# Optimization experiments

Measured on AMD Instinct MI355X. Metric: run time of the kernel, lower is better.

The kernel has to match this reference:

```python
import jax, jax.numpy as jnp
import numpy as np

ALPHA = 1.0
BETA = 2.0
GAMMA = 1.5  # PositionEffectFunction default (config.gamma is NOT passed through)
TEMPERATURE = 1.0


def position_matrix(L: int) -> jnp.ndarray:
    idx = jnp.arange(L, dtype=jnp.float32)
    dist = jnp.abs(idx[:, None] - idx[None, :]) / L  # normalized |i-j|/L
    base = jnp.exp(-BETA * dist)
    return ALPHA * (1.0 + GAMMA * base) / (1.0 + GAMMA)  # [L, L]


def setup_inputs() -> dict:
    key = jax.random.key(0)
    ks = jax.random.split(key, 10)
    B, S, D = 8, 2048, 1024
    std = 0.02
    return {
        "x": jax.random.normal(ks[0], (B, S, D), jnp.float32),
        "pos_emb": jax.random.normal(ks[1], (1, S, D), jnp.float32),
        "Wq": jax.random.normal(ks[2], (D, D), jnp.float32) * std,
        "bq": jax.random.normal(ks[3], (D,), jnp.float32) * std,
        "Wk": jax.random.normal(ks[4], (D, D), jnp.float32) * std,
        "bk": jax.random.normal(ks[5], (D,), jnp.float32) * std,
        "Wv": jax.random.normal(ks[6], (D, D), jnp.float32) * std,
        "bv": jax.random.normal(ks[7], (D,), jnp.float32) * std,
        "Wo": jax.random.normal(ks[8], (D, D), jnp.float32) * std,
        "bo": jax.random.normal(ks[9], (D,), jnp.float32) * std,
    }


def reference(x, pos_emb, Wq, bq, Wk, bk, Wv, bv, Wo, bo):
    B, S, D = x.shape
    x = x + pos_emb[:, :S, :]
    Q = x @ Wq + bq  # [B,S,D]
    K = x @ Wk + bk
    V = x @ Wv + bv
    scores = jnp.einsum("bsd,btd->bst", Q, K) / jnp.sqrt(jnp.float32(D))
    pw = position_matrix(S)  # [S,S], broadcast over batch
    scores = scores * pw[None, :, :] / TEMPERATURE
    attn = jax.nn.softmax(scores, axis=-1)  # [B,S,S]
    out = jnp.einsum("bst,btd->bsd", attn, V)
    out = out @ Wo + bo
    return out, attn
```

## Files before the change

kernel.cpp:

```cpp
#include <hip/hip_runtime.h>
#include <hip/hip_bf16.h>
#include <cstdint>

typedef _Float16 f16x8 __attribute__((ext_vector_type(8)));
typedef _Float16 f16x4 __attribute__((ext_vector_type(4)));
typedef float    f32x4 __attribute__((ext_vector_type(4)));

static constexpr int B = 8, S = 2048, D = 1024;
static constexpr long BSD = (long)B * S * D;
static constexpr long SD  = (long)S * D;
static constexpr long SS  = (long)S * S;
static constexpr long DD  = (long)D * D;

__device__ __forceinline__ void gload16(const void* g, void* l) {
  __builtin_amdgcn_global_load_lds(
      (const __attribute__((address_space(1))) void*)g,
      (__attribute__((address_space(3))) void*)l, 16, 0, 0);
}

#define CFENCE() asm volatile("" ::: "memory")

__global__ __launch_bounds__(256) void prep_x_kernel(
    const float* __restrict__ x, const float* __restrict__ pos,
    _Float16* __restrict__ xh) {
  long i = ((long)blockIdx.x * 256 + threadIdx.x) * 4;
  float4 xv = *(const float4*)(x + i);
  long p = i & (SD - 1);
  float4 pv = *(const float4*)(pos + p);
  f16x4 h;
  h.x = (_Float16)(xv.x + pv.x);
  h.y = (_Float16)(xv.y + pv.y);
  h.z = (_Float16)(xv.z + pv.z);
  h.w = (_Float16)(xv.w + pv.w);
  *(f16x4*)(xh + i) = h;
}

__global__ __launch_bounds__(256) void prep_w_kernel(
    const float* __restrict__ Wq, const float* __restrict__ Wk,
    const float* __restrict__ Wv, const float* __restrict__ Wo,
    _Float16* __restrict__ wqkv, _Float16* __restrict__ woh) {
  __shared__ _Float16 t[64][65];
  const int c0 = blockIdx.x * 64;
  const int r0 = blockIdx.y * 64;
  const int tid = threadIdx.x;
  const int lc = tid & 63;
  const int lr4 = tid >> 6;
  const float* srcs[4] = {Wq, Wk, Wv, Wo};
  #pragma unroll
  for (int m = 0; m < 4; ++m) {
    const float* src = srcs[m];
    _Float16* dst = (m < 3) ? (wqkv + (long)m * DD) : woh;
    #pragma unroll
    for (int ii = 0; ii < 16; ++ii) {
      int row = ii * 4 + lr4;
      t[lc][row] = (_Float16)src[(long)(r0 + row) * D + c0 + lc];
    }
    __syncthreads();
    #pragma unroll
    for (int ii = 0; ii < 16; ++ii) {
      int orow = ii * 4 + lr4;
      dst[(long)(c0 + orow) * D + r0 + lc] = t[orow][lc];
    }
    __syncthreads();
  }
}

__global__ __launch_bounds__(256) void prep_misc_kernel(
    const float* __restrict__ bq, const float* __restrict__ bk,
    const float* __restrict__ bv,
    float* __restrict__ bcat, float* __restrict__ pwtab) {
  int i = blockIdx.x * 256 + threadIdx.x;
  if (i < 3072) {
    float v = (i < 1024) ? bq[i] : (i < 2048) ? bk[i - 1024] : bv[i - 2048];
    bcat[i] = v;
  }
  int d = i - 3072;
  if (d >= 0 && d < 2048) {
    float dist = (float)d * (1.0f / 2048.0f);
    pwtab[d] = (1.0f + 1.5f * expf(-2.0f * dist)) * (1.0f / 2.5f) * (1.0f / 32.0f);
  }
}


enum { EPI_QKV = 0, EPI_SF16 = 1, EPI_PVO = 2, EPI_F32B = 3 };

__device__ __forceinline__ void stage_half(
    char* smem, const _Float16* mb, int off, int k64K, int sthb,
    int dst0, int dst1) {
  gload16(mb + off, smem + sthb + dst0);
  gload16(mb + off + k64K, smem + sthb + dst1);
}

__device__ __forceinline__ void rdA(const char* p, f16x8 (&af)[4][2]) {
#pragma unroll
  for (int mr = 0; mr < 4; ++mr)
#pragma unroll
    for (int kk = 0; kk < 2; ++kk)
      af[mr][kk] = *(const f16x8*)(p + mr * 2048 + kk * 1024);
}

__device__ __forceinline__ void rdB(const char* p, f16x8 (&bf)[2][2]) {
#pragma unroll
  for (int nr = 0; nr < 2; ++nr)
#pragma unroll
    for (int kk = 0; kk < 2; ++kk)
      bf[nr][kk] = *(const f16x8*)(p + nr * 2048 + kk * 1024);
}

__device__ __forceinline__ void mfma16(const f16x8 (&af)[4][2],
                                       const f16x8 (&bf)[2][2],
                                       f32x4 (&a4)[4][2]) {
#pragma unroll
  for (int kk = 0; kk < 2; ++kk)
#pragma unroll
    for (int mr = 0; mr < 4; ++mr)
#pragma unroll
      for (int nr = 0; nr < 2; ++nr)
        a4[mr][nr] = __builtin_amdgcn_mfma_f32_16x16x32_f16(
            af[mr][kk], bf[nr][kk], a4[mr][nr], 0, 0, 0);
}

template<int EPI>
__global__ __launch_bounds__(512, 2) void gemm256_kernel(
    const _Float16* __restrict__ A, const _Float16* __restrict__ Bt,
    const float* __restrict__ bias, const float* __restrict__ pwtab,
    float* __restrict__ outF,
    _Float16* __restrict__ o0, _Float16* __restrict__ o1, _Float16* __restrict__ o2,
    int M, int N, int K, long sA, long sB, long sC)
{
  __shared__ __align__(16) char smem[131072];
  const int tid = threadIdx.x;

  int bx = blockIdx.x, by = blockIdx.y, bz = blockIdx.z;
  if (gridDim.z == 1) {
    const int bid = by * gridDim.x + bx;
    const int idx = bid >> 3;
    by = ((bid & 7) << 3) + (idx & 7);
    bx = idx >> 3;
  } else {
    const int f = (bz * gridDim.y + by) * gridDim.x + bx;
    bz = f & 7;
    const int r = f >> 3;
    const int ri = r & 15;
    const int cid = r >> 4;
    const int cxs = gridDim.x >> 2;
    bx = (cid & (cxs - 1)) * 4 + (ri & 3);
    by = (cid / cxs) * 4 + (ri >> 2);
  }
  const int z = bz;
  const int rb = by * 256;
  const int cb = bx * 256;
  const _Float16* Ag = A + (long)z * sA + (long)rb * K;
  const _Float16* Bg = Bt + (long)z * sB + (long)cb * K;

  const int lane = tid & 63;
  const int wid = tid >> 6;
  const int lrin = lane & 15;
  const int lhi = lane >> 4;
  const int rtail = (lrin * 64 + lhi * 16) ^ (((lane >> 3) & 1) << 5);
  const int aoff = ((wid >> 2) * 4) * 2048 + rtail;
  const int boff = ((wid & 3) * 2) * 2048 + rtail;

  const int rin = lane >> 2;
  const int cinp = (lane & 3) ^ (((lane >> 5) & 1) << 1);
  const int rowc = (wid >> 1) * 16 + rin;
  const int colc = (wid & 1) * 32 + cinp * 8;
  const int stBase = rowc * K + colc;
  const int k64K = 64 * K;
  const int h128K = 128 * K;
  const int dst0 = tid * 16;
  const int dst1 = 8192 + tid * 16;

  const int NT = K >> 6;
  f32x4 acc00[4][2] = {}, acc01[4][2] = {}, acc11[4][2] = {}, acc10[4][2] = {};

  stage_half(smem, Ag, stBase,              k64K, 0,             dst0, dst1);
  stage_half(smem, Bg, stBase,              k64K, 32768,         dst0, dst1);
  stage_half(smem, Ag, stBase + h128K,      k64K, 16384,         dst0, dst1);
  stage_half(smem, Bg, stBase + h128K,      k64K, 49152,         dst0, dst1);
  stage_half(smem, Ag, stBase + 64,         k64K, 65536,         dst0, dst1);
  stage_half(smem, Bg, stBase + h128K + 64, k64K, 65536 + 49152, dst0, dst1);
  asm volatile("s_waitcnt vmcnt(4)" ::: "memory");
  __builtin_amdgcn_s_barrier();
  CFENCE();

  for (int t = 0; t < NT; ++t) {
    const int curbase = (t & 1) << 16;
    const int nxtbase = curbase ^ 65536;
    const bool s1ok = (t + 1) < NT;
    const bool s2ok = (t + 2) < NT;
    const int st1 = stBase + (t + 1) * 64;
    const int st2 = stBase + (t + 2) * 64;
    f16x8 af[4][2], bfA[2][2], bfB[2][2];

    rdA((const char*)smem + curbase + aoff, af);
    rdB((const char*)smem + curbase + 32768 + boff, bfA);
    if (s1ok) stage_half(smem, Ag, st1 + h128K, k64K, nxtbase + 16384, dst0, dst1);
    CFENCE();
    __builtin_amdgcn_s_barrier();
    CFENCE();
    __builtin_amdgcn_s_setprio(1);
    mfma16(af, bfA, acc00);
    __builtin_amdgcn_s_setprio(0);

    rdB((const char*)smem + curbase + 49152 + boff, bfB);
    if (s1ok) stage_half(smem, Bg, st1, k64K, nxtbase + 32768, dst0, dst1);
    CFENCE();
    __builtin_amdgcn_s_barrier();
    CFENCE();
    __builtin_amdgcn_s_setprio(1);
    mfma16(af, bfB, acc01);
    __builtin_amdgcn_s_setprio(0);

    rdA((const char*)smem + curbase + 16384 + aoff, af);
    if (s2ok) stage_half(smem, Ag, st2, k64K, curbase + 0, dst0, dst1);
    CFENCE();
    __builtin_amdgcn_s_barrier();
    CFENCE();
    __builtin_amdgcn_s_setprio(1);
    mfma16(af, bfB, acc11);
    __builtin_amdgcn_s_setprio(0);

    rdB((const char*)smem + curbase + 32768 + boff, bfA);
    if (s2ok) stage_half(smem, Bg, st2 + h128K, k64K, curbase + 49152, dst0, dst1);
    if (s2ok) {
      asm volatile("s_waitcnt vmcnt(4)" ::: "memory");
    } else {
      asm volatile("s_waitcnt vmcnt(0)" ::: "memory");
    }
    CFENCE();
    __builtin_amdgcn_s_barrier();
    CFENCE();
    __builtin_amdgcn_s_setprio(1);
    mfma16(af, bfA, acc10);
    __builtin_amdgcn_s_setprio(0);
  }

  const int wrow = (wid >> 2) * 64;
  const int wcol = (wid & 3) * 32;
  const int matid = (EPI == EPI_QKV) ? (cb >> 10) : 0;

  if (EPI == EPI_F32B) {
    auto epi = [&](const f32x4 (&a4)[4][2], int qm, int qn) {
#pragma unroll
      for (int nr = 0; nr < 2; ++nr) {
        const int col = cb + qn * 128 + wcol + nr * 16 + lrin;
        const float bv = bias[col];
#pragma unroll
        for (int mr = 0; mr < 4; ++mr) {
          const int rowb = rb + qm * 128 + wrow + mr * 16 + lhi * 4;
          const f32x4 v4 = a4[mr][nr];
#pragma unroll
          for (int r = 0; r < 4; ++r)
            outF[(long)(rowb + r) * N + col] = v4[r] + bv;
        }
      }
    };
    epi(acc00, 0, 0);
    epi(acc01, 0, 1);
    epi(acc11, 1, 1);
    epi(acc10, 1, 0);
  } else if (EPI == EPI_QKV && matid == 2) {
    __syncthreads();
    auto vfrag = [&](const f32x4 (&a4)[4][2], int qm, int qn) {
#pragma unroll
      for (int nr = 0; nr < 2; ++nr) {
        const int dl = qn * 128 + wcol + nr * 16 + lrin;
        const float bv = bias[cb + dl];
        const int xr = (dl & 7) << 4;
#pragma unroll
        for (int mr = 0; mr < 4; ++mr) {
          const int tl = qm * 128 + wrow + mr * 16 + lhi * 4;
          const f32x4 v4 = a4[mr][nr];
          f16x4 p;
          p[0] = (_Float16)(v4[0] + bv);
          p[1] = (_Float16)(v4[1] + bv);
          p[2] = (_Float16)(v4[2] + bv);
          p[3] = (_Float16)(v4[3] + bv);
          *(f16x4*)(smem + dl * 512 + ((tl * 2) ^ xr)) = p;
        }
      }
    };
    vfrag(acc00, 0, 0);
    vfrag(acc01, 0, 1);
    vfrag(acc11, 1, 1);
    vfrag(acc10, 1, 0);
    __syncthreads();
    const int t0 = rb & (S - 1);
    const int bbk = rb >> 11;
    const int lr5 = tid & 31;
    const int dr0 = tid >> 5;
#pragma unroll
    for (int pass = 0; pass < 16; ++pass) {
      const int dl = pass * 16 + dr0;
      const f16x8 vv = *(const f16x8*)(smem + dl * 512 + ((lr5 * 16) ^ ((dl & 7) << 4)));
      *(f16x8*)(o2 + (long)bbk * SD + (long)(cb - 2048 + dl) * S + t0 + lr5 * 8) = vv;
    }
  } else {
    __syncthreads();
    auto toLds = [&](const f32x4 (&a4)[4][2], int qm, int qn) {
#pragma unroll
      for (int nr = 0; nr < 2; ++nr) {
        const int cl = qn * 128 + wcol + nr * 16 + lrin;
        const float bv = (EPI == EPI_QKV) ? bias[cb + cl] : 0.0f;
#pragma unroll
        for (int mr = 0; mr < 4; ++mr) {
          const int tl0 = qm * 128 + wrow + mr * 16 + lhi * 4;
          const f32x4 v4 = a4[mr][nr];
#pragma unroll
          for (int r = 0; r < 4; ++r) {
            const int tl = tl0 + r;
            float v = v4[r];
            if (EPI == EPI_QKV) {
              v += bv;
            } else if (EPI == EPI_SF16) {
              int dd = (rb + tl) - (cb + cl); if (dd < 0) dd = -dd;
              v *= pwtab[dd];
            }
            *(_Float16*)(smem + tl * 512 + ((((cl >> 3) ^ (tl & 31))) << 4) + (cl & 7) * 2) =
                (_Float16)v;
          }
        }
      }
    };
    toLds(acc00, 0, 0);
    toLds(acc01, 0, 1);
    toLds(acc11, 1, 1);
    toLds(acc10, 1, 0);
    __syncthreads();
    const int lr5 = tid & 31;
    const int r0 = tid >> 5;
#pragma unroll
    for (int pass = 0; pass < 16; ++pass) {
      const int row = pass * 16 + r0;
      const f16x8 vv = *(const f16x8*)(smem + row * 512 + ((lr5 ^ (row & 31)) << 4));
      if (EPI == EPI_QKV) {
        _Float16* dst = matid ? o1 : o0;
        *(f16x8*)(dst + (long)(rb + row) * 1024 + (cb & 1023) + lr5 * 8) = vv;
      } else {
        *(f16x8*)(o0 + (long)z * sC + (long)(rb + row) * N + cb + lr5 * 8) = vv;
      }
    }
  }
}

__global__ __launch_bounds__(256) void softmax_kernel(
    const _Float16* __restrict__ sbf, float* __restrict__ attn,
    _Float16* __restrict__ abf) {
  const long base = (long)blockIdx.x * S + threadIdx.x * 8;
  const int tid = threadIdx.x;
  const f16x8 sv = *(const f16x8*)(sbf + base);
  float v[8];
  #pragma unroll
  for (int t = 0; t < 8; ++t) v[t] = (float)sv[t];
  float m = fmaxf(fmaxf(fmaxf(v[0], v[1]), fmaxf(v[2], v[3])),
                  fmaxf(fmaxf(v[4], v[5]), fmaxf(v[6], v[7])));
  #pragma unroll
  for (int sh = 1; sh < 64; sh <<= 1) m = fmaxf(m, __shfl_xor(m, sh));
  __shared__ float red[8];
  const int w = tid >> 6;
  if ((tid & 63) == 0) red[w] = m;
  __syncthreads();
  m = fmaxf(fmaxf(red[0], red[1]), fmaxf(red[2], red[3]));
  float e[8];
  #pragma unroll
  for (int t = 0; t < 8; ++t) e[t] = expf(v[t] - m);
  float s8 = ((e[0] + e[1]) + (e[2] + e[3])) + ((e[4] + e[5]) + (e[6] + e[7]));
  #pragma unroll
  for (int sh = 1; sh < 64; sh <<= 1) s8 += __shfl_xor(s8, sh);
  if ((tid & 63) == 0) red[4 + w] = s8;
  __syncthreads();
  const float inv = 1.0f / ((red[4] + red[5]) + (red[6] + red[7]));
  float4 o0 = make_float4(e[0] * inv, e[1] * inv, e[2] * inv, e[3] * inv);
  float4 o1 = make_float4(e[4] * inv, e[5] * inv, e[6] * inv, e[7] * inv);
  *(float4*)(attn + base) = o0;
  *(float4*)(attn + base + 4) = o1;
  f16x8 hb;
  hb[0] = (_Float16)o0.x; hb[1] = (_Float16)o0.y;
  hb[2] = (_Float16)o0.z; hb[3] = (_Float16)o0.w;
  hb[4] = (_Float16)o1.x; hb[5] = (_Float16)o1.y;
  hb[6] = (_Float16)o1.z; hb[7] = (_Float16)o1.w;
  *(f16x8*)(abf + base) = hb;
}

extern "C" void kernel_launch(void* const* d_in, const int* in_sizes, int n_in,
                              void* d_out, int out_size, void* d_ws, size_t ws_size,
                              hipStream_t stream) {
  const float* x   = (const float*)d_in[0];
  const float* pos = (const float*)d_in[1];
  const float* Wq  = (const float*)d_in[2];
  const float* bq  = (const float*)d_in[3];
  const float* Wk  = (const float*)d_in[4];
  const float* bk  = (const float*)d_in[5];
  const float* Wv  = (const float*)d_in[6];
  const float* bv  = (const float*)d_in[7];
  const float* Wo  = (const float*)d_in[8];
  const float* bo  = (const float*)d_in[9];

  float* outp  = (float*)d_out;
  float* attnp = outp + BSD;

  _Float16* wqkv = (_Float16*)d_ws;
  _Float16* woh  = wqkv + 3 * DD;
  float*    bcat = (float*)(woh + DD);
  float*    pwtab = bcat + 3072;
  _Float16* qh  = (_Float16*)(pwtab + 2048);
  _Float16* kh  = qh + BSD;
  _Float16* vt  = kh + BSD;
  _Float16* sbf = vt + BSD;
  _Float16* abf = sbf + (long)B * SS;
  _Float16* hbf = qh;

  _Float16* xph = (_Float16*)attnp;

  dim3 blk(256);
  prep_w_kernel<<<dim3(16, 16), blk, 0, stream>>>(Wq, Wk, Wv, Wo, wqkv, woh);
  prep_misc_kernel<<<dim3(20), blk, 0, stream>>>(bq, bk, bv, bcat, pwtab);
  prep_x_kernel<<<dim3((int)(BSD / 1024)), blk, 0, stream>>>(x, pos, xph);

  dim3 blk5(512);
  gemm256_kernel<EPI_QKV><<<dim3(12, 64, 1), blk5, 0, stream>>>(
      xph, wqkv, bcat, nullptr, nullptr, qh, kh, vt, B * S, 3 * D, D, 0, 0, 0);

  gemm256_kernel<EPI_SF16><<<dim3(8, 8, B), blk5, 0, stream>>>(
      qh, kh, nullptr, pwtab, nullptr, sbf, nullptr, nullptr, S, S, D, SD, SD, SS);

  softmax_kernel<<<dim3(B * S), blk, 0, stream>>>(sbf, attnp, abf);

  gemm256_kernel<EPI_PVO><<<dim3(4, 8, B), blk5, 0, stream>>>(
      abf, vt, nullptr, nullptr, nullptr, hbf, nullptr, nullptr, S, D, S, SS, SD, SD);

  gemm256_kernel<EPI_F32B><<<dim3(4, 64, 1), blk5, 0, stream>>>(
      hbf, woh, bo, nullptr, outp, nullptr, nullptr, nullptr, B * S, D, D, 0, 0, 0);
}
```

Baseline: 380.3 us.

## Restructure GEMM main loop into two phases with fewer barriers

The four-phase K-loop, with one barrier and one MFMA block per quadrant, becomes two phases. Each phase loads both B fragments into registers and issues two MFMA blocks, so each A fragment is used twice per barrier. Global-to-LDS stage copies are grouped at the start of each phase after an explicit lgkmcnt wait. This halves barrier count and LDS reloads of B, at the cost of more live registers and a different overlap of copies with compute. There is a possible hazard: stage writes into curbase regions that waves may still be reading during the phase.

```diff
diff --git a/kernel.cpp b/kernel.cpp
--- a/kernel.cpp
+++ b/kernel.cpp
@@ -191,48 +191,41 @@
     const bool s2ok = (t + 2) < NT;
     const int st1 = stBase + (t + 1) * 64;
     const int st2 = stBase + (t + 2) * 64;
-    f16x8 af[4][2], bfA[2][2], bfB[2][2];
-
+    f16x8 af[4][2], bf0[2][2], bf1[2][2];
+
+    asm volatile("s_waitcnt lgkmcnt(0)" ::: "memory");
+    if (s1ok) {
+      stage_half(smem, Ag, st1 + h128K, k64K, nxtbase + 16384, dst0, dst1);
+      stage_half(smem, Bg, st1,         k64K, nxtbase + 32768, dst0, dst1);
+    }
     rdA((const char*)smem + curbase + aoff, af);
-    rdB((const char*)smem + curbase + 32768 + boff, bfA);
-    if (s1ok) stage_half(smem, Ag, st1 + h128K, k64K, nxtbase + 16384, dst0, dst1);
+    rdB((const char*)smem + curbase + 32768 + boff, bf0);
+    rdB((const char*)smem + curbase + 49152 + boff, bf1);
     CFENCE();
     __builtin_amdgcn_s_barrier();
     CFENCE();
     __builtin_amdgcn_s_setprio(1);
-    mfma16(af, bfA, acc00);
+    mfma16(af, bf0, acc00);
+    mfma16(af, bf1, acc01);
     __builtin_amdgcn_s_setprio(0);
 
-    rdB((const char*)smem + curbase + 49152 + boff, bfB);
-    if (s1ok) stage_half(smem, Bg, st1, k64K, nxtbase + 32768, dst0, dst1);
+    asm volatile("s_waitcnt lgkmcnt(0)" ::: "memory");
+    if (s2ok) {
+      stage_half(smem, Ag, st2,         k64K, curbase + 0,     dst0, dst1);
+      stage_half(smem, Bg, st2 + h128K, k64K, curbase + 49152, dst0, dst1);
+    }
+    rdA((const char*)smem + curbase + 16384 + aoff, af);
+    if (s2ok) {
+      asm volatile("s_waitcnt vmcnt(4)" ::: "memory");
+    } else {
+      asm volatile("s_waitcnt vmcnt(0)" ::: "memory");
+    }
     CFENCE();
     __builtin_amdgcn_s_barrier();
     CFENCE();
     __builtin_amdgcn_s_setprio(1);
-    mfma16(af, bfB, acc01);
-    __builtin_amdgcn_s_setprio(0);
-
-    rdA((const char*)smem + curbase + 16384 + aoff, af);
-    if (s2ok) stage_half(smem, Ag, st2, k64K, curbase + 0, dst0, dst1);
-    CFENCE();
-    __builtin_amdgcn_s_barrier();
-    CFENCE();
-    __builtin_amdgcn_s_setprio(1);
-    mfma16(af, bfB, acc11);
-    __builtin_amdgcn_s_setprio(0);
-
-    rdB((const char*)smem + curbase + 32768 + boff, bfA);
-    if (s2ok) stage_half(smem, Bg, st2 + h128K, k64K, curbase + 49152, dst0, dst1);
-    if (s2ok) {
-      asm volatile("s_waitcnt vmcnt(4)" ::: "memory");
-    } else {
-      asm volatile("s_waitcnt vmcnt(0)" ::: "memory");
-    }
-    CFENCE();
-    __builtin_amdgcn_s_barrier();
-    CFENCE();
-    __builtin_amdgcn_s_setprio(1);
-    mfma16(af, bfA, acc10);
+    mfma16(af, bf1, acc11);
+    mfma16(af, bf0, acc10);
     __builtin_amdgcn_s_setprio(0);
   }
 
```

New measurement: 375.1 us, median of 2. Within noise of the previous version (-1.4%).
